# Performance work log

Hardware: AMD Instinct MI355X
Metric: run time of the kernel (lower is better)

## Reference

```python
import jax, jax.numpy as jnp
import numpy as np

K = 1024
D = 256
BETA = 0.25


def setup_inputs() -> dict:
    key = jax.random.key(0)
    kx, kc = jax.random.split(key)
    x = jax.random.normal(kx, (64, 32, 32, D), dtype=jnp.float32)
    limit = 1.0 / K
    codebook = jax.random.uniform(kc, (K, D), dtype=jnp.float32, minval=-limit, maxval=limit)
    return {"x": x, "codebook": codebook}


def reference(x, codebook):
    flat = x.reshape(-1, D)                                   # [N, D]
    x2 = jnp.sum(jnp.square(flat), axis=1, keepdims=True)     # [N, 1]
    e2 = jnp.sum(jnp.square(codebook), axis=1)                # [K]
    sim = flat @ codebook.T                                   # [N, K]
    dist = x2 + e2 - 2.0 * sim                                # [N, K]
    idx = jnp.argmin(dist, axis=1)                            # [N]
    q = codebook[idx].reshape(x.shape)                        # [..., D]

    q_st = jax.lax.stop_gradient(q)
    x_st = jax.lax.stop_gradient(x)
    commit = jnp.mean(jnp.square(q_st - x))
    codebk = jnp.mean(jnp.square(q - x_st))
    loss = BETA * commit + codebk

    # code-usage statistics via histogram (equivalent to mean of one-hot)
    counts = jnp.zeros((K,), dtype=x.dtype).at[idx].add(1.0)
    probs = counts / flat.shape[0]
    eps = jnp.asarray(1e-10, dtype=x.dtype)
    H = -jnp.sum(probs * jnp.log2(probs + eps))               # bits/index
    perplexity = jnp.exp(H * jnp.log(jnp.asarray(2.0, dtype=x.dtype)))
    usage = jnp.sum((probs > 0).astype(x.dtype)) / float(K)

    y = x + jax.lax.stop_gradient(q - x)                      # straight-through
    return y, idx, loss, perplexity, usage, H
```

## Files before the change

### kernel.cpp

```cpp
#include <hip/hip_runtime.h>
#include <math.h>

#define D       256
#define KCODES  1024
#define NROWS   65536
#define BETA    0.25f
#define MARGIN  3e-3f
#define MAXSURV 15

typedef __attribute__((ext_vector_type(8))) short bf16x8;
typedef __attribute__((ext_vector_type(4))) float f32x4;
typedef __attribute__((ext_vector_type(4))) int   i32x4;

__device__ __forceinline__ i32x4 mfma_i8(i32x4 a, i32x4 b, i32x4 c) {
    return __builtin_amdgcn_mfma_i32_16x16x64_i8(a, b, c, 0, 0, 0);
}
__device__ __forceinline__ int pack4(int a, int b, int c, int d) {
    return (a & 255) | ((b & 255) << 8) | ((c & 255) << 16) | (d << 24);
}

__global__ __launch_bounds__(256) void split_cb_kernel(const float* __restrict__ cb,
                                                       unsigned char* __restrict__ cs8,
                                                       float* __restrict__ e2f,
                                                       unsigned int* __restrict__ counts) {
    if (threadIdx.x < 4) counts[blockIdx.x * 4 + threadIdx.x] = 0u;
    int code = blockIdx.x * 4 + (threadIdx.x >> 6);
    int lane = threadIdx.x & 63;
    float4 v = ((const float4*)(cb + (size_t)code * D))[lane];
    double s = (double)v.x * v.x + (double)v.y * v.y +
               (double)v.z * v.z + (double)v.w * v.w;
    int q0 = __float2int_rn(v.x * 130048.0f);
    int q1 = __float2int_rn(v.y * 130048.0f);
    int q2 = __float2int_rn(v.z * 130048.0f);
    int q3 = __float2int_rn(v.w * 130048.0f);
    int d0 = lane * 4;
    int cp = d0 >> 5, qq = (d0 >> 3) & 3, j0 = d0 & 7;
    int p  = (cp >> 1) * 64 + qq * 16 + (cp & 1) * 8 + j0;
    *(int*)&cs8[(size_t)code * 256 + p] = pack4(q0, q1, q2, q3);
    #pragma unroll
    for (int off = 32; off > 0; off >>= 1) s += __shfl_down(s, off, 64);
    if (lane == 0) e2f[code] = (float)s;
}

__global__ __launch_bounds__(512, 4) void screen_kernel(
    const float* __restrict__ x, const unsigned char* __restrict__ cs8,
    const float* __restrict__ e2f, const float* __restrict__ cb,
    float* __restrict__ out_idxf, unsigned int* __restrict__ counts,
    float* __restrict__ y, float* __restrict__ msepart)
{
    __shared__ __attribute__((aligned(16))) char Bt[2][32 * 272];
    __shared__ unsigned mrg[128 * 33];
    __shared__ float x2s[128];
    __shared__ float sxn[128];
    #define MRG(r, j) mrg[(r) * 33 + (j)]

    const int tid  = threadIdx.x;
    const int wave = tid >> 6, lane = tid & 63;
    const int quad = lane >> 4, m = lane & 15;
    const int rowBase = blockIdx.x * 128;
    const int wrb = rowBase + wave * 16;

    const int sc = tid & 31, sp = tid >> 5;
    i32x4 stg;
    stg = *(const i32x4*)&cs8[(size_t)sc * 256 + sp * 16];

    const float* xr = x + (size_t)(wrb + m) * D;
    double s = 0.0;
    float amax = 0.0f;
    #pragma unroll
    for (int c = 0; c < 8; ++c) {
        float4 f0 = *(const float4*)&xr[c * 32 + quad * 8];
        float4 f1 = *(const float4*)&xr[c * 32 + quad * 8 + 4];
        s += (double)f0.x * f0.x + (double)f0.y * f0.y +
             (double)f0.z * f0.z + (double)f0.w * f0.w;
        s += (double)f1.x * f1.x + (double)f1.y * f1.y +
             (double)f1.z * f1.z + (double)f1.w * f1.w;
        amax = fmaxf(amax, fmaxf(fmaxf(fabsf(f0.x), fabsf(f0.y)),
                                 fmaxf(fabsf(f0.z), fabsf(f0.w))));
        amax = fmaxf(amax, fmaxf(fmaxf(fabsf(f1.x), fabsf(f1.y)),
                                 fmaxf(fabsf(f1.z), fabsf(f1.w))));
    }
    s += __shfl_xor(s, 16, 64);
    s += __shfl_xor(s, 32, 64);
    amax = fmaxf(amax, __shfl_xor(amax, 16, 64));
    amax = fmaxf(amax, __shfl_xor(amax, 32, 64));
    float rmax = fmaxf(amax, 1e-20f);
    float inv  = 127.0f / rmax;
    if (quad == 0) {
        x2s[wave * 16 + m] = (float)s;
        sxn[wave * 16 + m] = -2.0f * (rmax * (1.0f / 127.0f)) * (1.0f / 130048.0f);
    }

    i32x4 af[4];
    #pragma unroll
    for (int ck = 0; ck < 4; ++ck) {
        float4 a0 = *(const float4*)&xr[(2 * ck) * 32 + quad * 8];
        float4 a1 = *(const float4*)&xr[(2 * ck) * 32 + quad * 8 + 4];
        float4 b0 = *(const float4*)&xr[(2 * ck + 1) * 32 + quad * 8];
        float4 b1 = *(const float4*)&xr[(2 * ck + 1) * 32 + quad * 8 + 4];
        af[ck][0] = pack4(__float2int_rn(a0.x * inv), __float2int_rn(a0.y * inv),
                          __float2int_rn(a0.z * inv), __float2int_rn(a0.w * inv));
        af[ck][1] = pack4(__float2int_rn(a1.x * inv), __float2int_rn(a1.y * inv),
                          __float2int_rn(a1.z * inv), __float2int_rn(a1.w * inv));
        af[ck][2] = pack4(__float2int_rn(b0.x * inv), __float2int_rn(b0.y * inv),
                          __float2int_rn(b0.z * inv), __float2int_rn(b0.w * inv));
        af[ck][3] = pack4(__float2int_rn(b1.x * inv), __float2int_rn(b1.y * inv),
                          __float2int_rn(b1.z * inv), __float2int_rn(b1.w * inv));
    }

    unsigned u1[4], u2[4];
    #pragma unroll
    for (int r = 0; r < 4; ++r) { u1[r] = 0xFFFFFFFFu; u2[r] = 0xFFFFFFFFu; }

    *(i32x4*)&Bt[0][sc * 272 + sp * 16] = stg;
    __syncthreads();
    float sxr[4];
    #pragma unroll
    for (int r = 0; r < 4; ++r) sxr[r] = sxn[wave * 16 + quad * 4 + r];

    for (int kt = 0; kt < KCODES / 32; ++kt) {
        if (kt > 0) {
            *(i32x4*)&Bt[kt & 1][sc * 272 + sp * 16] = stg;
            __syncthreads();
        }
        if (kt < KCODES / 32 - 1)
            stg = *(const i32x4*)&cs8[(size_t)((kt + 1) * 32 + sc) * 256 + sp * 16];

        float e2pa = e2f[kt * 32 + m] + 0.5f;
        float e2pb = e2f[kt * 32 + 16 + m] + 0.5f;

        const char* Bcur = &Bt[kt & 1][0];
        #pragma unroll
        for (int nt = 0; nt < 2; ++nt) {
            i32x4 acc = {0, 0, 0, 0};
            const char* bp = Bcur + (nt * 16 + m) * 272 + quad * 16;
            __builtin_amdgcn_s_setprio(1);
            #pragma unroll
            for (int ck = 0; ck < 4; ++ck)
                acc = mfma_i8(af[ck], *(const i32x4*)(bp + ck * 64), acc);
            __builtin_amdgcn_s_setprio(0);
            unsigned kcode = kt * 32 + nt * 16 + m;
            float e2p = nt ? e2pb : e2pa;
            #pragma unroll
            for (int r = 0; r < 4; ++r) {
                float d = fmaf(sxr[r], (float)acc[r], e2p);
                unsigned u = (__float_as_uint(d) & 0xFFFFFC00u) | kcode;
                u2[r] = min(max(u, u1[r]), u2[r]);
                u1[r] = min(u, u1[r]);
            }
        }
    }

    #pragma unroll
    for (int r = 0; r < 4; ++r) {
        int rowloc = wave * 16 + quad * 4 + r;
        MRG(rowloc, m * 2 + 0) = u1[r];
        MRG(rowloc, m * 2 + 1) = u2[r];
    }
    __syncthreads();
    if (tid < 128) {
        unsigned umin = 0xFFFFFFFFu;
        #pragma unroll
        for (int j = 0; j < 32; ++j) umin = min(umin, MRG(tid, j));
        float dfloor = __uint_as_float(umin & 0xFFFFFC00u);
        unsigned limu = (__float_as_uint(dfloor + MARGIN) & 0xFFFFFC00u) | 1023u;
        ushort out[16];
        #pragma unroll
        for (int j = 0; j < 16; ++j) out[j] = 0;
        out[1] = (ushort)(umin & 1023u);
        int cnt = 1;
        for (int j = 0; j < 32; ++j) {
            unsigned u = MRG(tid, j);
            if (u <= limu && u != umin && cnt < MAXSURV) {
                out[1 + cnt] = (ushort)(u & 1023u); ++cnt;
            }
        }
        out[0] = (ushort)cnt;
        *(bf16x8*)&mrg[tid * 33]     = *(bf16x8*)&out[0];
        *(bf16x8*)&mrg[tid * 33 + 4] = *(bf16x8*)&out[8];
    }
    __syncthreads();

    #pragma unroll 2
    for (int i = 0; i < 16; ++i) {
        int rl  = wave * 16 + i;
        int row = rowBase + rl;
        const ushort* lst = (const ushort*)&mrg[rl * 33];
        int cnt = lst[0];
        float4 xv = ((const float4*)(x + (size_t)row * D))[lane];

        int bk;
        if (cnt == 1) {
            bk = lst[1];
        } else {
            float x2 = x2s[rl];
            float bestd = 1e30f;
            int   bestk = 0;
            for (int ss = 0; ss < cnt; ++ss) {
                int k = lst[1 + ss];
                float4 cv = ((const float4*)(cb + (size_t)k * D))[lane];
                double p = (double)xv.x * cv.x + (double)xv.y * cv.y +
                           (double)xv.z * cv.z + (double)xv.w * cv.w;
                #pragma unroll
                for (int off = 32; off > 0; off >>= 1) p += __shfl_down(p, off, 64);
                float simf = (float)p;
                float tt   = x2 + e2f[k];
                float dq   = tt - 2.0f * simf;
                if (dq < bestd || (dq == bestd && k < bestk)) { bestd = dq; bestk = k; }
            }
            bk = __shfl(bestk, 0, 64);
        }
        if (lane == 0) {
            out_idxf[row] = (float)bk;
            atomicAdd(&counts[bk], 1u);
        }
        float4 q = ((const float4*)(cb + (size_t)bk * D))[lane];
        float4 dv;
        dv.x = q.x - xv.x; dv.y = q.y - xv.y; dv.z = q.z - xv.z; dv.w = q.w - xv.w;
        float4 yv;
        yv.x = xv.x + dv.x; yv.y = xv.y + dv.y; yv.z = xv.z + dv.z; yv.w = xv.w + dv.w;
        ((float4*)(y + (size_t)row * D))[lane] = yv;
        float s2 = dv.x * dv.x + dv.y * dv.y + dv.z * dv.z + dv.w * dv.w;
        #pragma unroll
        for (int off = 32; off > 0; off >>= 1) s2 += __shfl_down(s2, off, 64);
        if (lane == 0) msepart[row] = s2;
    }
    #undef MRG
}

__global__ __launch_bounds__(1024) void stats_kernel(
    const unsigned int* __restrict__ counts, const float* __restrict__ msepart,
    float* __restrict__ outs)
{
    int t = threadIdx.x;
    float ms = 0.f;
    #pragma unroll
    for (int j = 0; j < 64; ++j) ms += msepart[t + 1024 * j];

    float p = (float)counts[t] * (1.0f / 65536.0f);
    float h = -p * log2f(p + 1e-10f);
    float u = (p > 0.f) ? 1.f : 0.f;
    #pragma unroll
    for (int off = 32; off > 0; off >>= 1) {
        h  += __shfl_down(h,  off, 64);
        u  += __shfl_down(u,  off, 64);
        ms += __shfl_down(ms, off, 64);
    }
    __shared__ float hs[16], us[16], mss[16];
    int lane = t & 63, w = t >> 6;
    if (lane == 0) { hs[w] = h; us[w] = u; mss[w] = ms; }
    __syncthreads();
    if (t == 0) {
        float H = 0.f, U = 0.f, M = 0.f;
        #pragma unroll
        for (int i = 0; i < 16; ++i) { H += hs[i]; U += us[i]; M += mss[i]; }
        float m = M * (1.0f / 16777216.0f);
        float loss = BETA * m + m;
        float perp = expf(H * 0.69314718055994530942f);
        outs[0] = loss;
        outs[1] = perp;
        outs[2] = U * (1.0f / 1024.0f);
        outs[3] = H;
    }
}

extern "C" void kernel_launch(void* const* d_in, const int* in_sizes, int n_in,
                              void* d_out, int out_size, void* d_ws, size_t ws_size,
                              hipStream_t stream) {
    const float* x  = (const float*)d_in[0];
    const float* cb = (const float*)d_in[1];
    float* out      = (float*)d_out;

    float* y        = out;
    float* out_idxf = out + 16777216;
    float* outs     = out + 16777216 + 65536;

    float*         e2f     = (float*)((char*)d_ws + 262144);
    unsigned int*  counts  = (unsigned int*)((char*)d_ws + 266240);
    unsigned char* cs8     = (unsigned char*)((char*)d_ws + 1318976);
    float*         msepart = (float*)((char*)d_ws + 1843264);

    split_cb_kernel<<<KCODES / 4, 256, 0, stream>>>(cb, cs8, e2f, counts);
    screen_kernel<<<NROWS / 128, 512, 0, stream>>>(x, cs8, e2f, cb,
                                                   out_idxf, counts, y, msepart);
    stats_kernel<<<1, 1024, 0, stream>>>(counts, msepart, outs);
}
```

Baseline: 198.8 us.

## Stage half the codebook in LDS and process 32 rows per wave

Each block now handles 256 rows, and each wave handles 32 rows as two MFMA A-tiles that share every B fragment read from LDS. The int8 codebook is staged in two halves of 512 codes (a large padded LDS buffer that also holds the merge scratch), with the second half prefetched into registers during the first. This removes the per-32-code double-buffer barrier and halves LDS B traffic per MFMA. In exchange, LDS use and register pressure (16 staged vectors plus doubled accumulators) limit the CU to about one block, and the grid halves to 256 blocks. That reduces latency hiding in the screening and rescoring phases.

```diff
diff --git a/kernel.cpp b/kernel.cpp
--- a/kernel.cpp
+++ b/kernel.cpp
@@ -7,6 +7,7 @@
 #define BETA    0.25f
 #define MARGIN  3e-3f
 #define MAXSURV 15
+#define CSP     264
 
 typedef __attribute__((ext_vector_type(8))) short bf16x8;
 typedef __attribute__((ext_vector_type(4))) float f32x4;
@@ -42,123 +43,158 @@
     if (lane == 0) e2f[code] = (float)s;
 }
 
-__global__ __launch_bounds__(512, 4) void screen_kernel(
+__global__ __launch_bounds__(512) void screen_kernel(
     const float* __restrict__ x, const unsigned char* __restrict__ cs8,
     const float* __restrict__ e2f, const float* __restrict__ cb,
     float* __restrict__ out_idxf, unsigned int* __restrict__ counts,
     float* __restrict__ y, float* __restrict__ msepart)
 {
-    __shared__ __attribute__((aligned(16))) char Bt[2][32 * 272];
-    __shared__ unsigned mrg[128 * 33];
-    __shared__ float x2s[128];
-    __shared__ float sxn[128];
+    __shared__ __attribute__((aligned(16))) char CS[512 * CSP];
+    __shared__ float x2s[256];
+    __shared__ float sxn[256];
+    unsigned* mrg = (unsigned*)&CS[0];
     #define MRG(r, j) mrg[(r) * 33 + (j)]
 
     const int tid  = threadIdx.x;
     const int wave = tid >> 6, lane = tid & 63;
     const int quad = lane >> 4, m = lane & 15;
-    const int rowBase = blockIdx.x * 128;
-    const int wrb = rowBase + wave * 16;
-
-    const int sc = tid & 31, sp = tid >> 5;
-    i32x4 stg;
-    stg = *(const i32x4*)&cs8[(size_t)sc * 256 + sp * 16];
-
-    const float* xr = x + (size_t)(wrb + m) * D;
-    double s = 0.0;
-    float amax = 0.0f;
-    #pragma unroll
-    for (int c = 0; c < 8; ++c) {
-        float4 f0 = *(const float4*)&xr[c * 32 + quad * 8];
-        float4 f1 = *(const float4*)&xr[c * 32 + quad * 8 + 4];
-        s += (double)f0.x * f0.x + (double)f0.y * f0.y +
-             (double)f0.z * f0.z + (double)f0.w * f0.w;
-        s += (double)f1.x * f1.x + (double)f1.y * f1.y +
-             (double)f1.z * f1.z + (double)f1.w * f1.w;
-        amax = fmaxf(amax, fmaxf(fmaxf(fabsf(f0.x), fabsf(f0.y)),
-                                 fmaxf(fabsf(f0.z), fabsf(f0.w))));
-        amax = fmaxf(amax, fmaxf(fmaxf(fabsf(f1.x), fabsf(f1.y)),
-                                 fmaxf(fabsf(f1.z), fabsf(f1.w))));
-    }
-    s += __shfl_xor(s, 16, 64);
-    s += __shfl_xor(s, 32, 64);
-    amax = fmaxf(amax, __shfl_xor(amax, 16, 64));
-    amax = fmaxf(amax, __shfl_xor(amax, 32, 64));
-    float rmax = fmaxf(amax, 1e-20f);
-    float inv  = 127.0f / rmax;
-    if (quad == 0) {
-        x2s[wave * 16 + m] = (float)s;
-        sxn[wave * 16 + m] = -2.0f * (rmax * (1.0f / 127.0f)) * (1.0f / 130048.0f);
-    }
-
-    i32x4 af[4];
-    #pragma unroll
-    for (int ck = 0; ck < 4; ++ck) {
-        float4 a0 = *(const float4*)&xr[(2 * ck) * 32 + quad * 8];
-        float4 a1 = *(const float4*)&xr[(2 * ck) * 32 + quad * 8 + 4];
-        float4 b0 = *(const float4*)&xr[(2 * ck + 1) * 32 + quad * 8];
-        float4 b1 = *(const float4*)&xr[(2 * ck + 1) * 32 + quad * 8 + 4];
-        af[ck][0] = pack4(__float2int_rn(a0.x * inv), __float2int_rn(a0.y * inv),
-                          __float2int_rn(a0.z * inv), __float2int_rn(a0.w * inv));
-        af[ck][1] = pack4(__float2int_rn(a1.x * inv), __float2int_rn(a1.y * inv),
-                          __float2int_rn(a1.z * inv), __float2int_rn(a1.w * inv));
-        af[ck][2] = pack4(__float2int_rn(b0.x * inv), __float2int_rn(b0.y * inv),
-                          __float2int_rn(b0.z * inv), __float2int_rn(b0.w * inv));
-        af[ck][3] = pack4(__float2int_rn(b1.x * inv), __float2int_rn(b1.y * inv),
-                          __float2int_rn(b1.z * inv), __float2int_rn(b1.w * inv));
-    }
-
-    unsigned u1[4], u2[4];
-    #pragma unroll
-    for (int r = 0; r < 4; ++r) { u1[r] = 0xFFFFFFFFu; u2[r] = 0xFFFFFFFFu; }
-
-    *(i32x4*)&Bt[0][sc * 272 + sp * 16] = stg;
-    __syncthreads();
-    float sxr[4];
-    #pragma unroll
-    for (int r = 0; r < 4; ++r) sxr[r] = sxn[wave * 16 + quad * 4 + r];
-
-    for (int kt = 0; kt < KCODES / 32; ++kt) {
-        if (kt > 0) {
-            *(i32x4*)&Bt[kt & 1][sc * 272 + sp * 16] = stg;
+    const int rowBase = blockIdx.x * 256;
+    const int wrb = rowBase + wave * 32;
+
+    const int scode = tid >> 4;
+    const int spart = tid & 15;
+
+    i32x4 stg[16];
+    #pragma unroll
+    for (int p = 0; p < 16; ++p)
+        stg[p] = *(const i32x4*)&cs8[(size_t)(p * 32 + scode) * 256 + spart * 16];
+
+    float inv[2];
+    #pragma unroll
+    for (int t = 0; t < 2; ++t) {
+        const float* xr = x + (size_t)(wrb + t * 16 + m) * D;
+        double s = 0.0;
+        float amax = 0.0f;
+        #pragma unroll
+        for (int c = 0; c < 8; ++c) {
+            float4 f0 = *(const float4*)&xr[c * 32 + quad * 8];
+            float4 f1 = *(const float4*)&xr[c * 32 + quad * 8 + 4];
+            s += (double)f0.x * f0.x + (double)f0.y * f0.y +
+                 (double)f0.z * f0.z + (double)f0.w * f0.w;
+            s += (double)f1.x * f1.x + (double)f1.y * f1.y +
+                 (double)f1.z * f1.z + (double)f1.w * f1.w;
+            amax = fmaxf(amax, fmaxf(fmaxf(fabsf(f0.x), fabsf(f0.y)),
+                                     fmaxf(fabsf(f0.z), fabsf(f0.w))));
+            amax = fmaxf(amax, fmaxf(fmaxf(fabsf(f1.x), fabsf(f1.y)),
+                                     fmaxf(fabsf(f1.z), fabsf(f1.w))));
+        }
+        s += __shfl_xor(s, 16, 64);
+        s += __shfl_xor(s, 32, 64);
+        amax = fmaxf(amax, __shfl_xor(amax, 16, 64));
+        amax = fmaxf(amax, __shfl_xor(amax, 32, 64));
+        float rmax = fmaxf(amax, 1e-20f);
+        inv[t] = 127.0f / rmax;
+        if (quad == 0) {
+            x2s[wave * 32 + t * 16 + m] = (float)s;
+            sxn[wave * 32 + t * 16 + m] =
+                -2.0f * (rmax * (1.0f / 127.0f)) * (1.0f / 130048.0f);
+        }
+    }
+
+    i32x4 af[2][4];
+    #pragma unroll
+    for (int t = 0; t < 2; ++t) {
+        const float* xr = x + (size_t)(wrb + t * 16 + m) * D;
+        float iv = inv[t];
+        #pragma unroll
+        for (int ck = 0; ck < 4; ++ck) {
+            float4 a0 = *(const float4*)&xr[(2 * ck) * 32 + quad * 8];
+            float4 a1 = *(const float4*)&xr[(2 * ck) * 32 + quad * 8 + 4];
+            float4 b0 = *(const float4*)&xr[(2 * ck + 1) * 32 + quad * 8];
+            float4 b1 = *(const float4*)&xr[(2 * ck + 1) * 32 + quad * 8 + 4];
+            af[t][ck][0] = pack4(__float2int_rn(a0.x * iv), __float2int_rn(a0.y * iv),
+                                 __float2int_rn(a0.z * iv), __float2int_rn(a0.w * iv));
+            af[t][ck][1] = pack4(__float2int_rn(a1.x * iv), __float2int_rn(a1.y * iv),
+                                 __float2int_rn(a1.z * iv), __float2int_rn(a1.w * iv));
+            af[t][ck][2] = pack4(__float2int_rn(b0.x * iv), __float2int_rn(b0.y * iv),
+                                 __float2int_rn(b0.z * iv), __float2int_rn(b0.w * iv));
+            af[t][ck][3] = pack4(__float2int_rn(b1.x * iv), __float2int_rn(b1.y * iv),
+                                 __float2int_rn(b1.z * iv), __float2int_rn(b1.w * iv));
+        }
+    }
+
+    #pragma unroll
+    for (int p = 0; p < 16; ++p)
+        *(i32x4*)&CS[(size_t)(p * 32 + scode) * CSP + spart * 16] = stg[p];
+    __syncthreads();
+    #pragma unroll
+    for (int p = 0; p < 16; ++p)
+        stg[p] = *(const i32x4*)&cs8[(size_t)(512 + p * 32 + scode) * 256 + spart * 16];
+
+    unsigned u1[2][4], u2[2][4];
+    #pragma unroll
+    for (int t = 0; t < 2; ++t)
+        #pragma unroll
+        for (int r = 0; r < 4; ++r) { u1[t][r] = 0xFFFFFFFFu; u2[t][r] = 0xFFFFFFFFu; }
+    float sxr[2][4];
+    #pragma unroll
+    for (int t = 0; t < 2; ++t)
+        #pragma unroll
+        for (int r = 0; r < 4; ++r) sxr[t][r] = sxn[wave * 32 + t * 16 + quad * 4 + r];
+
+    for (int h = 0; h < 2; ++h) {
+        if (h == 1) {
             __syncthreads();
-        }
-        if (kt < KCODES / 32 - 1)
-            stg = *(const i32x4*)&cs8[(size_t)((kt + 1) * 32 + sc) * 256 + sp * 16];
-
-        float e2pa = e2f[kt * 32 + m] + 0.5f;
-        float e2pb = e2f[kt * 32 + 16 + m] + 0.5f;
-
-        const char* Bcur = &Bt[kt & 1][0];
-        #pragma unroll
-        for (int nt = 0; nt < 2; ++nt) {
-            i32x4 acc = {0, 0, 0, 0};
-            const char* bp = Bcur + (nt * 16 + m) * 272 + quad * 16;
-            __builtin_amdgcn_s_setprio(1);
             #pragma unroll
-            for (int ck = 0; ck < 4; ++ck)
-                acc = mfma_i8(af[ck], *(const i32x4*)(bp + ck * 64), acc);
-            __builtin_amdgcn_s_setprio(0);
-            unsigned kcode = kt * 32 + nt * 16 + m;
-            float e2p = nt ? e2pb : e2pa;
+            for (int p = 0; p < 16; ++p)
+                *(i32x4*)&CS[(size_t)(p * 32 + scode) * CSP + spart * 16] = stg[p];
+            __syncthreads();
+        }
+        for (int ktl = 0; ktl < 16; ++ktl) {
+            const int kt = h * 16 + ktl;
+            float e2pa = e2f[kt * 32 + m] + 0.5f;
+            float e2pb = e2f[kt * 32 + 16 + m] + 0.5f;
             #pragma unroll
-            for (int r = 0; r < 4; ++r) {
-                float d = fmaf(sxr[r], (float)acc[r], e2p);
-                unsigned u = (__float_as_uint(d) & 0xFFFFFC00u) | kcode;
-                u2[r] = min(max(u, u1[r]), u2[r]);
-                u1[r] = min(u, u1[r]);
+            for (int nt = 0; nt < 2; ++nt) {
+                i32x4 acc0 = {0, 0, 0, 0};
+                i32x4 acc1 = {0, 0, 0, 0};
+                const char* bp = &CS[(ktl * 32 + nt * 16 + m) * CSP + quad * 16];
+                __builtin_amdgcn_s_setprio(1);
+                #pragma unroll
+                for (int ck = 0; ck < 4; ++ck) {
+                    i32x4 b = *(const i32x4*)(bp + ck * 64);
+                    acc0 = mfma_i8(af[0][ck], b, acc0);
+                    acc1 = mfma_i8(af[1][ck], b, acc1);
+                }
+                __builtin_amdgcn_s_setprio(0);
+                unsigned kcode = kt * 32 + nt * 16 + m;
+                float e2p = nt ? e2pb : e2pa;
+                #pragma unroll
+                for (int t = 0; t < 2; ++t) {
+                    i32x4 acc = t ? acc1 : acc0;
+                    #pragma unroll
+                    for (int r = 0; r < 4; ++r) {
+                        float d = fmaf(sxr[t][r], (float)acc[r], e2p);
+                        unsigned u = (__float_as_uint(d) & 0xFFFFFC00u) | kcode;
+                        u2[t][r] = min(max(u, u1[t][r]), u2[t][r]);
+                        u1[t][r] = min(u, u1[t][r]);
+                    }
+                }
             }
         }
     }
-
-    #pragma unroll
-    for (int r = 0; r < 4; ++r) {
-        int rowloc = wave * 16 + quad * 4 + r;
-        MRG(rowloc, m * 2 + 0) = u1[r];
-        MRG(rowloc, m * 2 + 1) = u2[r];
-    }
-    __syncthreads();
-    if (tid < 128) {
+    __syncthreads();
+
+    #pragma unroll
+    for (int t = 0; t < 2; ++t)
+        #pragma unroll
+        for (int r = 0; r < 4; ++r) {
+            int rowloc = wave * 32 + t * 16 + quad * 4 + r;
+            MRG(rowloc, m * 2 + 0) = u1[t][r];
+            MRG(rowloc, m * 2 + 1) = u2[t][r];
+        }
+    __syncthreads();
+    if (tid < 256) {
         unsigned umin = 0xFFFFFFFFu;
         #pragma unroll
         for (int j = 0; j < 32; ++j) umin = min(umin, MRG(tid, j));
@@ -182,8 +218,8 @@
     __syncthreads();
 
     #pragma unroll 2
-    for (int i = 0; i < 16; ++i) {
-        int rl  = wave * 16 + i;
+    for (int i = 0; i < 32; ++i) {
+        int rl  = wave * 32 + i;
         int row = rowBase + rl;
         const ushort* lst = (const ushort*)&mrg[rl * 33];
         int cnt = lst[0];
@@ -281,7 +317,7 @@
     float*         msepart = (float*)((char*)d_ws + 1843264);
 
     split_cb_kernel<<<KCODES / 4, 256, 0, stream>>>(cb, cs8, e2f, counts);
-    screen_kernel<<<NROWS / 128, 512, 0, stream>>>(x, cs8, e2f, cb,
+    screen_kernel<<<NROWS / 256, 512, 0, stream>>>(x, cs8, e2f, cb,
                                                    out_idxf, counts, y, msepart);
     stats_kernel<<<1, 1024, 0, stream>>>(counts, msepart, outs);
 }
```

After: 257.4 us. +29.4%, slower.
